# Performance work log

Hardware: AMD Instinct MI355X
Metric: run time of the kernel (lower is better)

Reference implementation:

```python
import jax, jax.numpy as jnp
import numpy as np

N_NODES = 50000
N_EDGES = 800000
D = 256

def setup_inputs() -> dict:
    key = jax.random.key(0)
    k1, k2, k3, k4 = jax.random.split(key, 4)
    x = jax.random.normal(k1, (N_NODES, D), dtype=jnp.float32)
    edge_index = jax.random.randint(k2, (2, N_EDGES), 0, N_NODES, dtype=jnp.int32)
    W = jax.random.normal(k3, (D, D), dtype=jnp.float32)  # nn.Linear weight [out, in]
    a = jax.random.normal(k4, (D,), dtype=jnp.float32)
    return {"x": x, "edge_index": edge_index, "W": W, "a": a}

def reference(x, edge_index, W, a):
    src = edge_index[0]  # [E]
    dst = edge_index[1]  # [E]
    xi = x[src]          # [E, D]
    xj = x[dst]          # [E, D]
    # per-edge scalar feature: ||x_i - x_j||_2
    edge_features = jnp.linalg.norm(xi - xj, axis=1)  # [E]
    # a @ (W(x_i) + W(x_j));  nn.Linear: W(x) = x @ W.T
    h = (xi + xj) @ W.T                               # [E, D]
    scores = jax.nn.leaky_relu(h @ a, negative_slope=0.2)  # [E]
    # global softmax over all edges (dim=0 in torch)
    attention_weights = jax.nn.softmax(scores, axis=0)     # [E]
    msg = (attention_weights * edge_features)[:, None] * xj  # [E, D]
    out = jax.ops.segment_sum(msg, src, num_segments=N_NODES)  # [N, D]
    return out
```

## Files before the change

kernel.cpp:

```cpp
#include <hip/hip_runtime.h>


#define D 256
#define CAP 16384
#define BAND 30.0f
#define KN_BLOCKS 2048
#define KB_THREADS 256
#define EPT 4

__device__ __forceinline__ unsigned enc_f(float f) {
    unsigned u = __float_as_uint(f);
    return (u & 0x80000000u) ? ~u : (u | 0x80000000u);
}
__device__ __forceinline__ float dec_f(unsigned u) {
    return __uint_as_float((u & 0x80000000u) ? (u & 0x7FFFFFFFu) : ~u);
}

__global__ __launch_bounds__(1024) void compute_v_kernel(
    const float* __restrict__ W, const float* __restrict__ a,
    float* __restrict__ v, unsigned* __restrict__ smax_enc,
    int* __restrict__ count) {
    __shared__ float vpart[1024];
    const int tid = threadIdx.x;
    if (tid == 0) { *smax_enc = 0u; *count = 0; }
    const int i = tid & (D - 1);
    const int c = tid >> 8;
    float s = 0.f;
#pragma unroll 8
    for (int k = c * 64; k < c * 64 + 64; ++k) s += W[(size_t)k * D + i] * a[k];
    vpart[tid] = s;
    __syncthreads();
    if (tid < D) v[tid] = vpart[tid] + vpart[tid + 256] + vpart[tid + 512] + vpart[tid + 768];
}

__global__ __launch_bounds__(256) void node_kernel(
    const float* __restrict__ x, const float* __restrict__ v,
    float* __restrict__ p, int N) {
    const int tid = threadIdx.x;
    const int lane = tid & 63;
    const int wv = tid >> 6;
    const float4 v4 = reinterpret_cast<const float4*>(v)[lane];
    const int g = blockIdx.x * 4 + wv;
    const int stride = gridDim.x * 4;
    const float4* x4 = reinterpret_cast<const float4*>(x);

    int n = g;
    for (; n + 3 * stride < N; n += 4 * stride) {
        float4 a0 = x4[(size_t)n * 64 + lane];
        float4 a1 = x4[(size_t)(n + stride) * 64 + lane];
        float4 a2 = x4[(size_t)(n + 2 * stride) * 64 + lane];
        float4 a3 = x4[(size_t)(n + 3 * stride) * 64 + lane];
        float s0 = a0.x * v4.x + a0.y * v4.y + a0.z * v4.z + a0.w * v4.w;
        float s1 = a1.x * v4.x + a1.y * v4.y + a1.z * v4.z + a1.w * v4.w;
        float s2 = a2.x * v4.x + a2.y * v4.y + a2.z * v4.z + a2.w * v4.w;
        float s3 = a3.x * v4.x + a3.y * v4.y + a3.z * v4.z + a3.w * v4.w;
#pragma unroll
        for (int off = 32; off > 0; off >>= 1) {
            s0 += __shfl_xor(s0, off, 64);
            s1 += __shfl_xor(s1, off, 64);
            s2 += __shfl_xor(s2, off, 64);
            s3 += __shfl_xor(s3, off, 64);
        }
        if (lane == 0) {
            p[n] = s0;
            p[n + stride] = s1;
            p[n + 2 * stride] = s2;
            p[n + 3 * stride] = s3;
        }
    }
    for (; n < N; n += stride) {
        float4 a0 = x4[(size_t)n * 64 + lane];
        float s0 = a0.x * v4.x + a0.y * v4.y + a0.z * v4.z + a0.w * v4.w;
#pragma unroll
        for (int off = 32; off > 0; off >>= 1) s0 += __shfl_xor(s0, off, 64);
        if (lane == 0) p[n] = s0;
    }
}

__global__ __launch_bounds__(KB_THREADS) void edge_kernel(
    const int* __restrict__ ei, const float* __restrict__ p,
    unsigned long long* __restrict__ cand, unsigned* __restrict__ smax_enc,
    int* __restrict__ count, int E) {
    __shared__ float sred[KB_THREADS];
    __shared__ unsigned curEnc;
    const int tid = threadIdx.x;

    const int base = blockIdx.x * (KB_THREADS * EPT);
    int eArr[EPT];
    float sArr[EPT];
    float lmax = -INFINITY;
#pragma unroll
    for (int k = 0; k < EPT; ++k) {
        const int e = base + k * KB_THREADS + tid;
        eArr[k] = e;
        float sc = -INFINITY;
        if (e < E) {
            const int sn = ei[e];
            const int dn = ei[E + e];
            const float t = p[sn] + p[dn];
            sc = t > 0.f ? t : 0.2f * t;
        }
        sArr[k] = sc;
        lmax = fmaxf(lmax, sc);
    }
    sred[tid] = lmax;
    __syncthreads();
    for (int st = 128; st > 0; st >>= 1) {
        if (tid < st) sred[tid] = fmaxf(sred[tid], sred[tid + st]);
        __syncthreads();
    }
    if (tid == 0) {
        const unsigned mine = enc_f(sred[0]);
        const unsigned old = atomicMax(smax_enc, mine);
        curEnc = old > mine ? old : mine;
    }
    __syncthreads();
    const float cur = dec_f(curEnc);
#pragma unroll
    for (int k = 0; k < EPT; ++k) {
        if (sArr[k] >= cur - BAND) {
            const int idx = atomicAdd(count, 1);
            if (idx < CAP) {
                cand[idx] = ((unsigned long long)__float_as_uint(sArr[k]) << 32) |
                            (unsigned)eArr[k];
            }
        }
    }
}

__global__ __launch_bounds__(KB_THREADS) void finalize_kernel(
    const float* __restrict__ x, const int* __restrict__ ei,
    const unsigned long long* __restrict__ cand,
    const unsigned* __restrict__ smax_enc, const int* __restrict__ count,
    float* __restrict__ out, int E) {
    __shared__ float sred[KB_THREADS];
    __shared__ int lcnt;
    __shared__ unsigned long long lsurv[256];

    const int tid = threadIdx.x;
    if (tid == 0) lcnt = 0;
    __syncthreads();

    const float smax = dec_f(*smax_enc);
    const int cnt = min(*count, CAP);
    float zpart = 0.f;
    for (int ci = tid; ci < cnt; ci += KB_THREADS) {
        const unsigned long long pk = cand[ci];
        const float sc = __uint_as_float((unsigned)(pk >> 32));
        const float w = expf(sc - smax);
        zpart += w;
        if (w >= 1e-10f) {
            const int li = atomicAdd(&lcnt, 1);
            if (li < 256) lsurv[li] = pk;
        }
    }
    sred[tid] = zpart;
    __syncthreads();
    for (int st = 128; st > 0; st >>= 1) {
        if (tid < st) sred[tid] += sred[tid + st];
        __syncthreads();
    }
    const float Zinv = 1.f / sred[0];
    const int ns = min(lcnt, 256);
    __syncthreads();
    for (int j = 0; j < ns; ++j) {
        const unsigned long long pk = lsurv[j];
        const int e = (int)(pk & 0xFFFFFFFFu);
        const float w = expf(__uint_as_float((unsigned)(pk >> 32)) - smax);
        const int sn = ei[e];
        const int dn = ei[E + e];
        const float xi = x[(size_t)sn * D + tid];
        const float xj = x[(size_t)dn * D + tid];
        const float df = xi - xj;
        sred[tid] = df * df;
        __syncthreads();
        for (int st = 128; st > 0; st >>= 1) {
            if (tid < st) sred[tid] += sred[tid + st];
            __syncthreads();
        }
        const float coef = w * Zinv * sqrtf(sred[0]);
        __syncthreads();
        atomicAdd(&out[(size_t)sn * D + tid], coef * xj);
    }
}

extern "C" void kernel_launch(void* const* d_in, const int* in_sizes, int n_in,
                              void* d_out, int out_size, void* d_ws, size_t ws_size,
                              hipStream_t stream) {
    const float* x  = (const float*)d_in[0];
    const int*   ei = (const int*)d_in[1];
    const float* W  = (const float*)d_in[2];
    const float* a  = (const float*)d_in[3];
    float* out = (float*)d_out;
    const int E = in_sizes[1] / 2;
    const int N = in_sizes[0] / D;

    float* ws = (float*)d_ws;
    float* v = ws;
    float* p = v + D;
    unsigned long long* cand =
        (unsigned long long*)(((uintptr_t)(p + N) + 7) & ~(uintptr_t)7);
    unsigned* smax_enc = (unsigned*)(cand + CAP);
    int* count = (int*)(smax_enc + 1);

    compute_v_kernel<<<1, 1024, 0, stream>>>(W, a, v, smax_enc, count);
    node_kernel<<<KN_BLOCKS, 256, 0, stream>>>(x, v, p, N);
    const int GB = (E + KB_THREADS * EPT - 1) / (KB_THREADS * EPT);
    edge_kernel<<<GB, KB_THREADS, 0, stream>>>(ei, p, cand, smax_enc, count, E);
    finalize_kernel<<<1, KB_THREADS, 0, stream>>>(x, ei, cand, smax_enc, count, out, E);
}
```

Measured before the change: 124.9 us.

## Fuse edge scoring and finalize via last-block completion counter

Merges the edge scoring kernel and the single-block finalize kernel into one launch: each block bumps a global done counter, and the last block to finish performs the softmax normalization and scatter. Edge indices are now read as int4 vectors with each thread owning four consecutive edges. This removes one kernel launch and its inter-kernel gap, at the cost of atomic reads for cross-block visibility and a serialized tail inside the last block.

```diff
diff --git a/kernel.cpp b/kernel.cpp
--- a/kernel.cpp
+++ b/kernel.cpp
@@ -15,14 +15,17 @@
 __device__ __forceinline__ float dec_f(unsigned u) {
     return __uint_as_float((u & 0x80000000u) ? (u & 0x7FFFFFFFu) : ~u);
 }
+__device__ __forceinline__ float leaky(float t) {
+    return t > 0.f ? t : 0.2f * t;
+}
 
 __global__ __launch_bounds__(1024) void compute_v_kernel(
     const float* __restrict__ W, const float* __restrict__ a,
     float* __restrict__ v, unsigned* __restrict__ smax_enc,
-    int* __restrict__ count) {
+    int* __restrict__ count, int* __restrict__ done) {
     __shared__ float vpart[1024];
     const int tid = threadIdx.x;
-    if (tid == 0) { *smax_enc = 0u; *count = 0; }
+    if (tid == 0) { *smax_enc = 0u; *count = 0; *done = 0; }
     const int i = tid & (D - 1);
     const int c = tid >> 8;
     float s = 0.f;
@@ -77,32 +80,40 @@
     }
 }
 
-__global__ __launch_bounds__(KB_THREADS) void edge_kernel(
-    const int* __restrict__ ei, const float* __restrict__ p,
-    unsigned long long* __restrict__ cand, unsigned* __restrict__ smax_enc,
-    int* __restrict__ count, int E) {
+__global__ __launch_bounds__(KB_THREADS) void edge_finalize_kernel(
+    const float* __restrict__ x, const int* __restrict__ ei,
+    const float* __restrict__ p, unsigned long long* __restrict__ cand,
+    unsigned* __restrict__ smax_enc, int* __restrict__ count,
+    int* __restrict__ done, float* __restrict__ out, int E) {
     __shared__ float sred[KB_THREADS];
     __shared__ unsigned curEnc;
+    __shared__ int lastFlag;
+    __shared__ int lcnt;
+    __shared__ unsigned long long lsurv[256];
+
     const int tid = threadIdx.x;
-
     const int base = blockIdx.x * (KB_THREADS * EPT);
-    int eArr[EPT];
+    const int eBase = base + tid * EPT;
     float sArr[EPT];
     float lmax = -INFINITY;
-#pragma unroll
-    for (int k = 0; k < EPT; ++k) {
-        const int e = base + k * KB_THREADS + tid;
-        eArr[k] = e;
-        float sc = -INFINITY;
-        if (e < E) {
-            const int sn = ei[e];
-            const int dn = ei[E + e];
-            const float t = p[sn] + p[dn];
-            sc = t > 0.f ? t : 0.2f * t;
-        }
-        sArr[k] = sc;
-        lmax = fmaxf(lmax, sc);
-    }
+
+    if (base + KB_THREADS * EPT <= E) {
+        const int4 s4 = reinterpret_cast<const int4*>(ei)[(base >> 2) + tid];
+        const int4 d4 = reinterpret_cast<const int4*>(ei + E)[(base >> 2) + tid];
+        sArr[0] = leaky(p[s4.x] + p[d4.x]);
+        sArr[1] = leaky(p[s4.y] + p[d4.y]);
+        sArr[2] = leaky(p[s4.z] + p[d4.z]);
+        sArr[3] = leaky(p[s4.w] + p[d4.w]);
+    } else {
+#pragma unroll
+        for (int k = 0; k < EPT; ++k) {
+            const int e = eBase + k;
+            sArr[k] = (e < E) ? leaky(p[ei[e]] + p[ei[E + e]]) : -INFINITY;
+        }
+    }
+#pragma unroll
+    for (int k = 0; k < EPT; ++k) lmax = fmaxf(lmax, sArr[k]);
+
     sred[tid] = lmax;
     __syncthreads();
     for (int st = 128; st > 0; st >>= 1) {
@@ -121,31 +132,30 @@
         if (sArr[k] >= cur - BAND) {
             const int idx = atomicAdd(count, 1);
             if (idx < CAP) {
-                cand[idx] = ((unsigned long long)__float_as_uint(sArr[k]) << 32) |
-                            (unsigned)eArr[k];
+                const unsigned long long pk =
+                    ((unsigned long long)__float_as_uint(sArr[k]) << 32) |
+                    (unsigned)(eBase + k);
+                atomicExch(&cand[idx], pk);
             }
         }
     }
-}
-
-__global__ __launch_bounds__(KB_THREADS) void finalize_kernel(
-    const float* __restrict__ x, const int* __restrict__ ei,
-    const unsigned long long* __restrict__ cand,
-    const unsigned* __restrict__ smax_enc, const int* __restrict__ count,
-    float* __restrict__ out, int E) {
-    __shared__ float sred[KB_THREADS];
-    __shared__ int lcnt;
-    __shared__ unsigned long long lsurv[256];
-
-    const int tid = threadIdx.x;
-    if (tid == 0) lcnt = 0;
-    __syncthreads();
-
-    const float smax = dec_f(*smax_enc);
-    const int cnt = min(*count, CAP);
+    __threadfence_block();
+    __syncthreads();
+    if (tid == 0) {
+        const int d = __hip_atomic_fetch_add(done, 1, __ATOMIC_RELAXED,
+                                             __HIP_MEMORY_SCOPE_AGENT);
+        lastFlag = (d == (int)gridDim.x - 1);
+        lcnt = 0;
+    }
+    __syncthreads();
+    if (!lastFlag) return;
+
+    const float smax = dec_f(atomicAdd(smax_enc, 0u));
+    int cnt = atomicAdd(count, 0);
+    cnt = min(cnt, CAP);
     float zpart = 0.f;
     for (int ci = tid; ci < cnt; ci += KB_THREADS) {
-        const unsigned long long pk = cand[ci];
+        const unsigned long long pk = atomicAdd(&cand[ci], 0ULL);
         const float sc = __uint_as_float((unsigned)(pk >> 32));
         const float w = expf(sc - smax);
         zpart += w;
@@ -202,10 +212,11 @@
         (unsigned long long*)(((uintptr_t)(p + N) + 7) & ~(uintptr_t)7);
     unsigned* smax_enc = (unsigned*)(cand + CAP);
     int* count = (int*)(smax_enc + 1);
-
-    compute_v_kernel<<<1, 1024, 0, stream>>>(W, a, v, smax_enc, count);
+    int* done = count + 1;
+
+    compute_v_kernel<<<1, 1024, 0, stream>>>(W, a, v, smax_enc, count, done);
     node_kernel<<<KN_BLOCKS, 256, 0, stream>>>(x, v, p, N);
     const int GB = (E + KB_THREADS * EPT - 1) / (KB_THREADS * EPT);
-    edge_kernel<<<GB, KB_THREADS, 0, stream>>>(ei, p, cand, smax_enc, count, E);
-    finalize_kernel<<<1, KB_THREADS, 0, stream>>>(x, ei, cand, smax_enc, count, out, E);
-}
+    edge_finalize_kernel<<<GB, KB_THREADS, 0, stream>>>(
+        x, ei, p, cand, smax_enc, count, done, out, E);
+}
```

After: 134.1 us. 7.3% more time.
